# Kernel tuning notes

Hardware: AMD Instinct MI355X
Metric: run time of the kernel (lower is better)

The kernel has to match this reference:

```python
import jax, jax.numpy as jnp
import numpy as np

F = 128          # nbr_fea_len
A = 64           # angle_fea_len
N_EDGES = 100_000
N_ANGLES = 400_000
N_CRYST = 512
EPS = 1e-5
INV_SQRT_2 = 1.0 / 2.0 ** 0.5


def layer_norm(x, g, b):
    mu = jnp.mean(x, axis=-1, keepdims=True)
    var = jnp.var(x, axis=-1, keepdims=True)
    return (x - mu) * jax.lax.rsqrt(var + EPS) * g + b


def setup_inputs() -> dict:
    key = jax.random.key(0)
    ks = jax.random.split(key, 16)
    def lin(k, out_f, in_f):
        return (jax.random.normal(k, (out_f, in_f), jnp.float32) * (1.0 / np.sqrt(in_f))).astype(jnp.float32)
    return {
        "nbr_fea": jax.random.normal(ks[0], (N_EDGES, F), jnp.float32),
        "angle_fea": jax.random.normal(ks[1], (N_ANGLES, A), jnp.float32),
        "angle_nbr_idx": jax.random.randint(ks[2], (N_ANGLES, 2), 0, N_EDGES),
        "crystal_edge_idx": jax.random.randint(ks[3], (N_EDGES,), 0, N_CRYST),
        "crystal_angle_index": jnp.sort(jax.random.randint(ks[4], (N_ANGLES,), 0, N_CRYST)),
        "W_full": lin(ks[5], 2 * F, 2 * F + A),
        "W_mask": lin(ks[6], 1, F),
        "cn_gamma": jnp.ones((2 * F,), jnp.float32),
        "cn_beta": jnp.zeros((2 * F,), jnp.float32),
        "ln_core_g": jnp.ones((F,), jnp.float32),
        "ln_core_b": jnp.zeros((F,), jnp.float32),
        "ln2_g": jnp.ones((F,), jnp.float32),
        "ln2_b": jnp.zeros((F,), jnp.float32),
        "res_W1a": lin(ks[7], F // 2, F), "res_b1a": jnp.zeros((F // 2,), jnp.float32),
        "res_W2a": lin(ks[8], F, F // 2), "res_b2a": jnp.zeros((F,), jnp.float32),
        "res_W1b": lin(ks[9], F // 2, F), "res_b1b": jnp.zeros((F // 2,), jnp.float32),
        "res_W2b": lin(ks[10], F, F // 2), "res_b2b": jnp.zeros((F,), jnp.float32),
    }


def reference(nbr_fea, angle_fea, angle_nbr_idx, crystal_edge_idx, crystal_angle_index,
              W_full, W_mask, cn_gamma, cn_beta, ln_core_g, ln_core_b, ln2_g, ln2_b,
              res_W1a, res_b1a, res_W2a, res_b2a, res_W1b, res_b1b, res_W2b, res_b2b):
    source_idx = angle_nbr_idx[:, 0]
    # gather the two neighbor edge features per angle -> [n_angles, 2F]
    pair = nbr_fea[angle_nbr_idx].reshape(-1, 2 * F)
    total = jnp.concatenate([angle_fea, pair], axis=1)          # [n_angles, 2F+A]
    h = total @ W_full.T                                        # [n_angles, 2F]

    # Crystal_Norm: per-crystal, per-feature normalization over angle rows
    seg = crystal_angle_index
    cnt = jnp.maximum(jax.ops.segment_sum(jnp.ones((h.shape[0], 1), h.dtype), seg, N_CRYST), 1.0)
    mean = jax.ops.segment_sum(h, seg, N_CRYST) / cnt
    diff = h - mean[seg]
    var = jax.ops.segment_sum(diff * diff, seg, N_CRYST) / cnt
    h = diff * jax.lax.rsqrt(var + EPS)[seg] * cn_gamma + cn_beta

    nbr_core, nbr_filter = h[:, :F], h[:, F:]
    nbr_core = jax.nn.silu(layer_norm(nbr_core, ln_core_g, ln_core_b))
    gate = jax.nn.sigmoid(nbr_filter @ W_mask.T)                # [n_angles, 1]
    msg = gate * nbr_core

    # scatter-mean over source edge; empty edges get 0 (matches scatter+pad)
    s = jax.ops.segment_sum(msg, source_idx, N_EDGES)
    c = jax.ops.segment_sum(jnp.ones((msg.shape[0], 1), msg.dtype), source_idx, N_EDGES)
    nbr_sumed = s / jnp.maximum(c, 1.0)

    x = layer_norm(nbr_sumed, ln2_g, ln2_b)
    # two residual bottleneck blocks: x + fc2(silu(fc1(x)))
    x = x + (jax.nn.silu(x @ res_W1a.T + res_b1a) @ res_W2a.T + res_b2a)
    x = x + (jax.nn.silu(x @ res_W1b.T + res_b1b) @ res_W2b.T + res_b2b)
    return INV_SQRT_2 * (nbr_fea + x)
```

## Files before the change

kernel.cpp:

```cpp
#include <hip/hip_runtime.h>
#include <hip/hip_bf16.h>
#include <cstdint>
#include <cstddef>

#define NF 128
#define N_EDGES 100000
#define N_ANGLES 400000
#define N_CRYST 512
#define KDIM 320
#define TWOF 256
#define EPS_LN 1e-5f
#define INV_SQRT_2 0.70710678118654752440f

typedef short short8 __attribute__((ext_vector_type(8)));
typedef float floatx4 __attribute__((ext_vector_type(4)));

__device__ inline unsigned short f2bf(float x) {
    __hip_bfloat16 b = __float2bfloat16(x);
    return *reinterpret_cast<unsigned short*>(&b);
}
__device__ inline float bf2f(__hip_bfloat16 b) { return __bfloat162float(b); }
__device__ inline float bfbits2f(unsigned short u) {
    unsigned int v = ((unsigned int)u) << 16;
    return __uint_as_float(v);
}

__device__ inline uint4 cvt8(float4 a, float4 b) {
    __hip_bfloat162 p0 = __float22bfloat162_rn(make_float2(a.x, a.y));
    __hip_bfloat162 p1 = __float22bfloat162_rn(make_float2(a.z, a.w));
    __hip_bfloat162 p2 = __float22bfloat162_rn(make_float2(b.x, b.y));
    __hip_bfloat162 p3 = __float22bfloat162_rn(make_float2(b.z, b.w));
    uint4 r;
    r.x = *reinterpret_cast<unsigned int*>(&p0);
    r.y = *reinterpret_cast<unsigned int*>(&p1);
    r.z = *reinterpret_cast<unsigned int*>(&p2);
    r.w = *reinterpret_cast<unsigned int*>(&p3);
    return r;
}

__global__ void seg_bounds(const int* __restrict__ seg, int* __restrict__ seg_start) {
    int s = blockIdx.x * blockDim.x + threadIdx.x;
    if (s > N_CRYST) return;
    if (s == N_CRYST) { seg_start[N_CRYST] = N_ANGLES; return; }
    int lo = 0, hi = N_ANGLES;
    while (lo < hi) { int mid = (lo + hi) >> 1; if (seg[mid] < s) lo = mid + 1; else hi = mid; }
    seg_start[s] = lo;
}

__global__ __launch_bounds__(512) void gemm_gather_mfma(
    const float* __restrict__ angle_fea,
    const float* __restrict__ nbr_fea,
    const int*   __restrict__ angle_nbr_idx,
    const float* __restrict__ W_full,
    __hip_bfloat16* __restrict__ hout)
{
    __shared__ uint4 X_lds[512];
    __shared__ uint4 W_lds[1024];

    const int tid  = threadIdx.x;
    const int row0 = blockIdx.x * 128;

    const int xm = tid >> 2;
    const int xk = ((tid & 3) ^ ((xm >> 1) & 3)) * 8;
    const int p0 = angle_nbr_idx[(size_t)(row0 + xm) * 2 + 0];
    const int p1 = angle_nbr_idx[(size_t)(row0 + xm) * 2 + 1];
    int wn[2], wk[2];
    #pragma unroll
    for (int it = 0; it < 2; ++it) {
        int tau = it * 512 + tid;
        wn[it] = tau >> 2;
        wk[it] = ((tau & 3) ^ ((wn[it] >> 1) & 3)) * 8;
    }

    const int wave = tid >> 6, lane = tid & 63;
    const int wrow = (wave & 1) * 64;
    const int wcol = (wave >> 1) * 64;
    const int rl   = lane & 15, kgrp = lane >> 4;
    const int fragoff = (kgrp ^ ((rl >> 1) & 3)) * 16;
    const char* Xb = (const char*)X_lds;
    const char* Wb = (const char*)W_lds;

    floatx4 acc[4][4];
    #pragma unroll
    for (int i = 0; i < 4; ++i)
        #pragma unroll
        for (int j = 0; j < 4; ++j)
            acc[i][j] = (floatx4){0.f, 0.f, 0.f, 0.f};

    float4 xa, xb2, wa0, wb0, wa1, wb1;
    auto loadX = [&](int kbase, float4& a, float4& b) {
        const float* src;
        if (kbase < 64)       src = angle_fea + (size_t)(row0 + xm) * 64 + kbase + xk;
        else if (kbase < 192) src = nbr_fea + (size_t)p0 * 128 + (kbase - 64) + xk;
        else                  src = nbr_fea + (size_t)p1 * 128 + (kbase - 192) + xk;
        a = ((const float4*)src)[0];
        b = ((const float4*)src)[1];
    };
    auto loadW = [&](int kbase, int it, float4& a, float4& b) {
        const float* src = W_full + (size_t)wn[it] * KDIM + kbase + wk[it];
        a = ((const float4*)src)[0];
        b = ((const float4*)src)[1];
    };

    loadX(0, xa, xb2);
    loadW(0, 0, wa0, wb0);
    loadW(0, 1, wa1, wb1);

    #pragma unroll
    for (int kiter = 0; kiter < 10; ++kiter) {
        uint4 xc  = cvt8(xa, xb2);
        uint4 wc0 = cvt8(wa0, wb0);
        uint4 wc1 = cvt8(wa1, wb1);
        if (kiter > 0) __syncthreads();
        X_lds[tid]       = xc;
        W_lds[tid]       = wc0;
        W_lds[512 + tid] = wc1;
        __syncthreads();
        if (kiter < 9) {
            int nb = (kiter + 1) * 32;
            loadX(nb, xa, xb2);
            loadW(nb, 0, wa0, wb0);
            loadW(nb, 1, wa1, wb1);
        }
        short8 wf[4], xf[4];
        #pragma unroll
        for (int i = 0; i < 4; ++i)
            wf[i] = *(const short8*)(Wb + (size_t)(wcol + i * 16 + rl) * 64 + fragoff);
        #pragma unroll
        for (int j = 0; j < 4; ++j)
            xf[j] = *(const short8*)(Xb + (size_t)(wrow + j * 16 + rl) * 64 + fragoff);
        #pragma unroll
        for (int i = 0; i < 4; ++i)
            #pragma unroll
            for (int j = 0; j < 4; ++j)
                acc[i][j] = __builtin_amdgcn_mfma_f32_16x16x32_bf16(wf[i], xf[j], acc[i][j], 0, 0, 0);
    }

    unsigned short* hp = reinterpret_cast<unsigned short*>(hout);
    #pragma unroll
    for (int j = 0; j < 4; ++j) {
        size_t r = (size_t)(row0 + wrow + j * 16 + rl);
        #pragma unroll
        for (int i = 0; i < 4; ++i) {
            int c = wcol + i * 16 + kgrp * 4;
            floatx4 v = acc[i][j];
            uint2 pk;
            pk.x = (unsigned int)f2bf(v[0]) | ((unsigned int)f2bf(v[1]) << 16);
            pk.y = (unsigned int)f2bf(v[2]) | ((unsigned int)f2bf(v[3]) << 16);
            *reinterpret_cast<uint2*>(hp + r * TWOF + c) = pk;
        }
    }
}

__global__ __launch_bounds__(256) void seg_stats(
    const __hip_bfloat16* __restrict__ h,
    const int* __restrict__ seg_start,
    float* __restrict__ segSum, float* __restrict__ segSumSq)
{
    __shared__ float redS[8][256];
    __shared__ float redQ[8][256];
    int seg   = blockIdx.x;
    int split = blockIdx.y;
    int start = seg_start[seg], end = seg_start[seg + 1];
    int n = end - start;
    int g = threadIdx.x >> 5, t = threadIdx.x & 31;
    float s[8] = {0.f,0.f,0.f,0.f,0.f,0.f,0.f,0.f};
    float q[8] = {0.f,0.f,0.f,0.f,0.f,0.f,0.f,0.f};
    if (n > 0) {
        int per = (n + 3) >> 2;
        int r0 = start + split * per;
        int r1 = min(r0 + per, end);
        const unsigned short* hp = (const unsigned short*)h;
        for (int r = r0 + g; r < r1; r += 8) {
            uint4 v = *(const uint4*)(hp + (size_t)r * TWOF + t * 8);
            unsigned int d[4] = {v.x, v.y, v.z, v.w};
            #pragma unroll
            for (int i = 0; i < 4; ++i) {
                float lo = __uint_as_float(d[i] << 16);
                float hi = __uint_as_float(d[i] & 0xffff0000u);
                s[2*i]   += lo; q[2*i]   += lo * lo;
                s[2*i+1] += hi; q[2*i+1] += hi * hi;
            }
        }
    }
    #pragma unroll
    for (int i = 0; i < 8; ++i) { redS[g][t * 8 + i] = s[i]; redQ[g][t * 8 + i] = q[i]; }
    __syncthreads();
    if (n > 0) {
        int col = threadIdx.x;
        float S = 0.f, Q = 0.f;
        #pragma unroll
        for (int gg = 0; gg < 8; ++gg) { S += redS[gg][col]; Q += redQ[gg][col]; }
        atomicAdd(&segSum[seg * TWOF + col], S);
        atomicAdd(&segSumSq[seg * TWOF + col], Q);
    }
}

__global__ __launch_bounds__(256) void seg_finalize(
    const int* __restrict__ seg_start,
    float* __restrict__ segSum, float* __restrict__ segSumSq)
{
    int seg = blockIdx.x;
    int j = threadIdx.x;
    float cnt = (float)max(seg_start[seg + 1] - seg_start[seg], 1);
    float inv = 1.0f / cnt;
    float mean = segSum[seg * TWOF + j] * inv;
    float var  = segSumSq[seg * TWOF + j] * inv - mean * mean;
    segSum[seg * TWOF + j]   = mean;
    segSumSq[seg * TWOF + j] = rsqrtf(var + EPS_LN);
}

__global__ __launch_bounds__(256) void angle_msg(
    const __hip_bfloat16* __restrict__ h,
    const int* __restrict__ seg_idx,
    const int* __restrict__ angle_nbr_idx,
    const float* __restrict__ segMean, const float* __restrict__ segScale,
    const float* __restrict__ cn_gamma, const float* __restrict__ cn_beta,
    const float* __restrict__ ln_g, const float* __restrict__ ln_b,
    const float* __restrict__ w_mask,
    float* __restrict__ s_acc, float* __restrict__ c_acc)
{
    int row  = blockIdx.x * 4 + (threadIdx.x >> 6);
    int lane = threadIdx.x & 63;
    int seg  = seg_idx[row];
    int src  = angle_nbr_idx[(size_t)row * 2];

    const __hip_bfloat16* hr = h + (size_t)row * TWOF;
    float y[4];
    #pragma unroll
    for (int qq = 0; qq < 4; ++qq) {
        int col = lane + qq * 64;
        float v = bf2f(hr[col]);
        float m = segMean[seg * TWOF + col], sc = segScale[seg * TWOF + col];
        y[qq] = (v - m) * sc * cn_gamma[col] + cn_beta[col];
    }
    float sum = y[0] + y[1], ssq = y[0] * y[0] + y[1] * y[1];
    #pragma unroll
    for (int o = 32; o > 0; o >>= 1) { sum += __shfl_xor(sum, o, 64); ssq += __shfl_xor(ssq, o, 64); }
    float mu  = sum * (1.f / 128.f);
    float var = ssq * (1.f / 128.f) - mu * mu;
    float rs  = rsqrtf(var + EPS_LN);
    float ln0 = (y[0] - mu) * rs * ln_g[lane]      + ln_b[lane];
    float ln1 = (y[1] - mu) * rs * ln_g[lane + 64] + ln_b[lane + 64];
    float si0 = ln0 / (1.f + __expf(-ln0));
    float si1 = ln1 / (1.f + __expf(-ln1));
    float gp = y[2] * w_mask[lane] + y[3] * w_mask[lane + 64];
    #pragma unroll
    for (int o = 32; o > 0; o >>= 1) gp += __shfl_xor(gp, o, 64);
    float gate = 1.f / (1.f + __expf(-gp));

    atomicAdd(&s_acc[(size_t)src * NF + lane],      gate * si0);
    atomicAdd(&s_acc[(size_t)src * NF + lane + 64], gate * si1);
    if (lane == 0) atomicAdd(&c_acc[src], 1.0f);
}

#define MT 64
#define XBS 136
#define H1S 72
#define W1S 136
#define W2S 72
__global__ __launch_bounds__(256) void edge_mlp_mfma(
    const float* __restrict__ s_acc, const float* __restrict__ c_acc,
    const float* __restrict__ nbr_fea,
    const float* __restrict__ ln2_g, const float* __restrict__ ln2_b,
    const float* __restrict__ W1a, const float* __restrict__ b1a,
    const float* __restrict__ W2a, const float* __restrict__ b2a,
    const float* __restrict__ W1b, const float* __restrict__ b1b,
    const float* __restrict__ W2b, const float* __restrict__ b2b,
    float* __restrict__ out)
{
    __shared__ unsigned short xb[MT * XBS];
    __shared__ unsigned short h1[MT * H1S];
    __shared__ unsigned short wl[128 * W2S];

    const int tid  = threadIdx.x;
    const int row0 = blockIdx.x * MT;
    const int w    = tid >> 6, lane = tid & 63;
    const int rl   = lane & 15, kgrp = lane >> 4;

    {
        int m = tid >> 2;
        int q = tid & 3;
        int e = min(row0 + m, N_EDGES - 1);
        float inv = 1.f / fmaxf(c_acc[e], 1.f);
        const float4* src = (const float4*)(s_acc + (size_t)e * NF + q * 32);
        float v[32];
        float sum = 0.f, ssq = 0.f;
        #pragma unroll
        for (int t = 0; t < 8; ++t) {
            float4 f = src[t];
            v[4*t+0] = f.x * inv; v[4*t+1] = f.y * inv; v[4*t+2] = f.z * inv; v[4*t+3] = f.w * inv;
        }
        #pragma unroll
        for (int i = 0; i < 32; ++i) { sum += v[i]; ssq += v[i] * v[i]; }
        sum += __shfl_xor(sum, 1, 64); ssq += __shfl_xor(ssq, 1, 64);
        sum += __shfl_xor(sum, 2, 64); ssq += __shfl_xor(ssq, 2, 64);
        float mu  = sum * (1.f / 128.f);
        float var = ssq * (1.f / 128.f) - mu * mu;
        float rs  = rsqrtf(var + EPS_LN);
        #pragma unroll
        for (int i = 0; i < 32; ++i) {
            int col = q * 32 + i;
            v[i] = (v[i] - mu) * rs * ln2_g[col] + ln2_b[col];
        }
        #pragma unroll
        for (int t = 0; t < 4; ++t) {
            float4 a = make_float4(v[8*t+0], v[8*t+1], v[8*t+2], v[8*t+3]);
            float4 b = make_float4(v[8*t+4], v[8*t+5], v[8*t+6], v[8*t+7]);
            *(uint4*)&xb[m * XBS + q * 32 + t * 8] = cvt8(a, b);
        }
    }

    const float* W1s[2] = {W1a, W1b};
    const float* B1s[2] = {b1a, b1b};
    const float* W2s[2] = {W2a, W2b};
    const float* B2s[2] = {b2a, b2b};

    #pragma unroll 1
    for (int blk = 0; blk < 2; ++blk) {
        const float* W1 = W1s[blk]; const float* B1 = B1s[blk];
        const float* W2 = W2s[blk]; const float* B2 = B2s[blk];

        __syncthreads();
        #pragma unroll
        for (int c = tid; c < 1024; c += 256) {
            int nn = c >> 4, kc = c & 15;
            const float* src = W1 + (size_t)nn * 128 + kc * 8;
            *(uint4*)&wl[nn * W1S + kc * 8] =
                cvt8(((const float4*)src)[0], ((const float4*)src)[1]);
        }
        __syncthreads();

        short8 xf[4];
        #pragma unroll
        for (int ks = 0; ks < 4; ++ks)
            xf[ks] = *(const short8*)&xb[(w * 16 + rl) * XBS + ks * 32 + kgrp * 8];
        floatx4 a1[4];
        #pragma unroll
        for (int i = 0; i < 4; ++i) {
            a1[i] = (floatx4){0.f, 0.f, 0.f, 0.f};
            #pragma unroll
            for (int ks = 0; ks < 4; ++ks) {
                short8 wf = *(const short8*)&wl[(i * 16 + rl) * W1S + ks * 32 + kgrp * 8];
                a1[i] = __builtin_amdgcn_mfma_f32_16x16x32_bf16(wf, xf[ks], a1[i], 0, 0, 0);
            }
        }
        #pragma unroll
        for (int i = 0; i < 4; ++i) {
            int nb = i * 16 + kgrp * 4;
            float s0 = a1[i][0] + B1[nb + 0];
            float s1 = a1[i][1] + B1[nb + 1];
            float s2 = a1[i][2] + B1[nb + 2];
            float s3 = a1[i][3] + B1[nb + 3];
            s0 = s0 / (1.f + __expf(-s0));
            s1 = s1 / (1.f + __expf(-s1));
            s2 = s2 / (1.f + __expf(-s2));
            s3 = s3 / (1.f + __expf(-s3));
            unsigned int lo = (unsigned int)f2bf(s0) | ((unsigned int)f2bf(s1) << 16);
            unsigned int hi = (unsigned int)f2bf(s2) | ((unsigned int)f2bf(s3) << 16);
            *(unsigned int*)&h1[(w * 16 + rl) * H1S + nb]     = lo;
            *(unsigned int*)&h1[(w * 16 + rl) * H1S + nb + 2] = hi;
        }

        __syncthreads();
        #pragma unroll
        for (int c = tid; c < 1024; c += 256) {
            int pp = c >> 3, kc = c & 7;
            const float* src = W2 + (size_t)pp * 64 + kc * 8;
            *(uint4*)&wl[pp * W2S + kc * 8] =
                cvt8(((const float4*)src)[0], ((const float4*)src)[1]);
        }
        __syncthreads();

        short8 hf[2];
        #pragma unroll
        for (int ks = 0; ks < 2; ++ks)
            hf[ks] = *(const short8*)&h1[(w * 16 + rl) * H1S + ks * 32 + kgrp * 8];
        #pragma unroll
        for (int p = 0; p < 8; ++p) {
            floatx4 a2 = (floatx4){0.f, 0.f, 0.f, 0.f};
            #pragma unroll
            for (int ks = 0; ks < 2; ++ks) {
                short8 wf = *(const short8*)&wl[(p * 16 + rl) * W2S + ks * 32 + kgrp * 8];
                a2 = __builtin_amdgcn_mfma_f32_16x16x32_bf16(wf, hf[ks], a2, 0, 0, 0);
            }
            int m = w * 16 + rl;
            #pragma unroll
            for (int reg = 0; reg < 4; ++reg) {
                int pcol = p * 16 + kgrp * 4 + reg;
                int idx  = m * XBS + pcol;
                float xv = bfbits2f(xb[idx]);
                xb[idx] = f2bf(xv + a2[reg] + B2[pcol]);
            }
        }
    }

    {
        int m = tid >> 2;
        int q = tid & 3;
        int e = row0 + m;
        if (e < N_EDGES) {
            const float4* nf = (const float4*)(nbr_fea + (size_t)e * NF + q * 32);
            float4* dst      = (float4*)(out + (size_t)e * NF + q * 32);
            #pragma unroll
            for (int t = 0; t < 8; ++t) {
                float4 f = nf[t];
                int col = q * 32 + 4 * t;
                dst[t] = make_float4(
                    INV_SQRT_2 * (f.x + bfbits2f(xb[m * XBS + col + 0])),
                    INV_SQRT_2 * (f.y + bfbits2f(xb[m * XBS + col + 1])),
                    INV_SQRT_2 * (f.z + bfbits2f(xb[m * XBS + col + 2])),
                    INV_SQRT_2 * (f.w + bfbits2f(xb[m * XBS + col + 3])));
            }
        }
    }
}


extern "C" void kernel_launch(void* const* d_in, const int* in_sizes, int n_in,
                              void* d_out, int out_size, void* d_ws, size_t ws_size,
                              hipStream_t stream) {
    const float* nbr_fea       = (const float*)d_in[0];
    const float* angle_fea     = (const float*)d_in[1];
    const int*   angle_nbr_idx = (const int*)d_in[2];
    const int*   cai           = (const int*)d_in[4];
    const float* W_full        = (const float*)d_in[5];
    const float* W_mask        = (const float*)d_in[6];
    const float* cn_gamma      = (const float*)d_in[7];
    const float* cn_beta       = (const float*)d_in[8];
    const float* ln_core_g     = (const float*)d_in[9];
    const float* ln_core_b     = (const float*)d_in[10];
    const float* ln2_g         = (const float*)d_in[11];
    const float* ln2_b         = (const float*)d_in[12];
    const float* W1a           = (const float*)d_in[13];
    const float* b1a           = (const float*)d_in[14];
    const float* W2a           = (const float*)d_in[15];
    const float* b2a           = (const float*)d_in[16];
    const float* W1b           = (const float*)d_in[17];
    const float* b1b           = (const float*)d_in[18];
    const float* W2b           = (const float*)d_in[19];
    const float* b2b           = (const float*)d_in[20];
    float* out = (float*)d_out;

    char* ws = (char*)d_ws;
    float* segSum    = (float*)(ws + 0);
    float* segSumSq  = (float*)(ws + 524288);
    float* s_acc     = (float*)(ws + 1048576);
    float* c_acc     = (float*)(ws + 52248576);
    int*   seg_start = (int*)  (ws + 52648576);
    __hip_bfloat16* h = (__hip_bfloat16*)(ws + 52652672);

    hipMemsetAsync(ws, 0, 52648576, stream);

    seg_bounds<<<3, 256, 0, stream>>>(cai, seg_start);
    gemm_gather_mfma<<<N_ANGLES / 128, 512, 0, stream>>>(
        angle_fea, nbr_fea, angle_nbr_idx, W_full, h);
    seg_stats<<<dim3(N_CRYST, 4), 256, 0, stream>>>(h, seg_start, segSum, segSumSq);
    seg_finalize<<<N_CRYST, 256, 0, stream>>>(seg_start, segSum, segSumSq);
    angle_msg<<<N_ANGLES / 4, 256, 0, stream>>>(
        h, cai, angle_nbr_idx, segSum, segSumSq,
        cn_gamma, cn_beta, ln_core_g, ln_core_b, W_mask, s_acc, c_acc);
    edge_mlp_mfma<<<(N_EDGES + MT - 1) / MT, 256, 0, stream>>>(
        s_acc, c_acc, nbr_fea, ln2_g, ln2_b,
        W1a, b1a, W2a, b2a, W1b, b1b, W2b, b2b, out);
}
```

Before: 689.7 us.

## Prepack W to bf16, preload gathered X tile, double-buffer W in GEMM

Adds a small kernel that converts W_full to swizzled bf16 once per call, so the GEMM no longer converts weights in every block. The GEMM now uses 64-row tiles with 256 threads. Each block loads and converts its whole gathered X tile (all K) into LDS up front, then streams prepacked W through a double-buffered LDS slot with one barrier per k-step. Separately, angle_msg is vectorized: each lane reads 4 bf16 values and float4 parameters, and the LayerNorm and gate reductions are split across half-waves. The cost is more LDS per block, which may lower occupancy, and W traffic doubles relative to the number of rows.

```diff
diff --git a/kernel.cpp b/kernel.cpp
--- a/kernel.cpp
+++ b/kernel.cpp
@@ -38,6 +38,17 @@
     return r;
 }
 
+__global__ __launch_bounds__(256) void w_pack(const float* __restrict__ W_full,
+                                              uint4* __restrict__ wsW) {
+    int s  = blockIdx.x * 256 + threadIdx.x;
+    int ki = s >> 10;
+    int sl = s & 1023;
+    int n  = sl >> 2, kc = sl & 3;
+    int ko = (kc ^ ((n >> 1) & 3)) * 8;
+    const float* src = W_full + (size_t)n * KDIM + ki * 32 + ko;
+    wsW[s] = cvt8(((const float4*)src)[0], ((const float4*)src)[1]);
+}
+
 __global__ void seg_bounds(const int* __restrict__ seg, int* __restrict__ seg_start) {
     int s = blockIdx.x * blockDim.x + threadIdx.x;
     if (s > N_CRYST) return;
@@ -47,38 +58,53 @@
     seg_start[s] = lo;
 }
 
-__global__ __launch_bounds__(512) void gemm_gather_mfma(
+__global__ __launch_bounds__(256) void gemm_gather_mfma(
     const float* __restrict__ angle_fea,
     const float* __restrict__ nbr_fea,
     const int*   __restrict__ angle_nbr_idx,
-    const float* __restrict__ W_full,
+    const uint4* __restrict__ wsW,
     __hip_bfloat16* __restrict__ hout)
 {
-    __shared__ uint4 X_lds[512];
-    __shared__ uint4 W_lds[1024];
+    __shared__ uint4 X_lds[2560];
+    __shared__ uint4 W_lds[2][1024];
 
     const int tid  = threadIdx.x;
-    const int row0 = blockIdx.x * 128;
+    const int row0 = blockIdx.x * 64;
 
     const int xm = tid >> 2;
-    const int xk = ((tid & 3) ^ ((xm >> 1) & 3)) * 8;
+    const int xko = ((tid & 3) ^ ((xm >> 1) & 3)) * 8;
     const int p0 = angle_nbr_idx[(size_t)(row0 + xm) * 2 + 0];
     const int p1 = angle_nbr_idx[(size_t)(row0 + xm) * 2 + 1];
-    int wn[2], wk[2];
-    #pragma unroll
-    for (int it = 0; it < 2; ++it) {
-        int tau = it * 512 + tid;
-        wn[it] = tau >> 2;
-        wk[it] = ((tau & 3) ^ ((wn[it] >> 1) & 3)) * 8;
-    }
+
+    float4 ra[10], rb[10];
+    #pragma unroll
+    for (int ki = 0; ki < 10; ++ki) {
+        const int kb = ki * 32;
+        const float* src;
+        if (kb < 64)       src = angle_fea + (size_t)(row0 + xm) * 64 + kb + xko;
+        else if (kb < 192) src = nbr_fea + (size_t)p0 * 128 + (kb - 64) + xko;
+        else               src = nbr_fea + (size_t)p1 * 128 + (kb - 192) + xko;
+        ra[ki] = ((const float4*)src)[0];
+        rb[ki] = ((const float4*)src)[1];
+    }
+    #pragma unroll
+    for (int ki = 0; ki < 10; ++ki)
+        X_lds[ki * 256 + tid] = cvt8(ra[ki], rb[ki]);
+
+    {
+        uint4 w0[4];
+        #pragma unroll
+        for (int it = 0; it < 4; ++it) w0[it] = wsW[it * 256 + tid];
+        #pragma unroll
+        for (int it = 0; it < 4; ++it) W_lds[0][it * 256 + tid] = w0[it];
+    }
+    __syncthreads();
 
     const int wave = tid >> 6, lane = tid & 63;
-    const int wrow = (wave & 1) * 64;
-    const int wcol = (wave >> 1) * 64;
+    const int wcol = wave * 64;
     const int rl   = lane & 15, kgrp = lane >> 4;
     const int fragoff = (kgrp ^ ((rl >> 1) & 3)) * 16;
     const char* Xb = (const char*)X_lds;
-    const char* Wb = (const char*)W_lds;
 
     floatx4 acc[4][4];
     #pragma unroll
@@ -87,59 +113,39 @@
         for (int j = 0; j < 4; ++j)
             acc[i][j] = (floatx4){0.f, 0.f, 0.f, 0.f};
 
-    float4 xa, xb2, wa0, wb0, wa1, wb1;
-    auto loadX = [&](int kbase, float4& a, float4& b) {
-        const float* src;
-        if (kbase < 64)       src = angle_fea + (size_t)(row0 + xm) * 64 + kbase + xk;
-        else if (kbase < 192) src = nbr_fea + (size_t)p0 * 128 + (kbase - 64) + xk;
-        else                  src = nbr_fea + (size_t)p1 * 128 + (kbase - 192) + xk;
-        a = ((const float4*)src)[0];
-        b = ((const float4*)src)[1];
-    };
-    auto loadW = [&](int kbase, int it, float4& a, float4& b) {
-        const float* src = W_full + (size_t)wn[it] * KDIM + kbase + wk[it];
-        a = ((const float4*)src)[0];
-        b = ((const float4*)src)[1];
-    };
-
-    loadX(0, xa, xb2);
-    loadW(0, 0, wa0, wb0);
-    loadW(0, 1, wa1, wb1);
-
-    #pragma unroll
-    for (int kiter = 0; kiter < 10; ++kiter) {
-        uint4 xc  = cvt8(xa, xb2);
-        uint4 wc0 = cvt8(wa0, wb0);
-        uint4 wc1 = cvt8(wa1, wb1);
-        if (kiter > 0) __syncthreads();
-        X_lds[tid]       = xc;
-        W_lds[tid]       = wc0;
-        W_lds[512 + tid] = wc1;
-        __syncthreads();
-        if (kiter < 9) {
-            int nb = (kiter + 1) * 32;
-            loadX(nb, xa, xb2);
-            loadW(nb, 0, wa0, wb0);
-            loadW(nb, 1, wa1, wb1);
-        }
+    #pragma unroll
+    for (int ki = 0; ki < 10; ++ki) {
+        uint4 wnext[4];
+        if (ki < 9) {
+            #pragma unroll
+            for (int it = 0; it < 4; ++it)
+                wnext[it] = wsW[(ki + 1) * 1024 + it * 256 + tid];
+        }
+        const char* Wb = (const char*)&W_lds[ki & 1][0];
         short8 wf[4], xf[4];
         #pragma unroll
         for (int i = 0; i < 4; ++i)
             wf[i] = *(const short8*)(Wb + (size_t)(wcol + i * 16 + rl) * 64 + fragoff);
         #pragma unroll
         for (int j = 0; j < 4; ++j)
-            xf[j] = *(const short8*)(Xb + (size_t)(wrow + j * 16 + rl) * 64 + fragoff);
+            xf[j] = *(const short8*)(Xb + (size_t)ki * 4096 + (size_t)(j * 16 + rl) * 64 + fragoff);
         #pragma unroll
         for (int i = 0; i < 4; ++i)
             #pragma unroll
             for (int j = 0; j < 4; ++j)
                 acc[i][j] = __builtin_amdgcn_mfma_f32_16x16x32_bf16(wf[i], xf[j], acc[i][j], 0, 0, 0);
+        if (ki < 9) {
+            #pragma unroll
+            for (int it = 0; it < 4; ++it)
+                W_lds[(ki + 1) & 1][it * 256 + tid] = wnext[it];
+            __syncthreads();
+        }
     }
 
     unsigned short* hp = reinterpret_cast<unsigned short*>(hout);
     #pragma unroll
     for (int j = 0; j < 4; ++j) {
-        size_t r = (size_t)(row0 + wrow + j * 16 + rl);
+        size_t r = (size_t)(row0 + j * 16 + rl);
         #pragma unroll
         for (int i = 0; i < 4; ++i) {
             int c = wcol + i * 16 + kgrp * 4;
@@ -224,34 +230,60 @@
     int lane = threadIdx.x & 63;
     int seg  = seg_idx[row];
     int src  = angle_nbr_idx[(size_t)row * 2];
-
-    const __hip_bfloat16* hr = h + (size_t)row * TWOF;
+    int c4   = lane * 4;
+
+    uint2 hv = *(const uint2*)((const unsigned short*)h + (size_t)row * TWOF + c4);
     float y[4];
-    #pragma unroll
-    for (int qq = 0; qq < 4; ++qq) {
-        int col = lane + qq * 64;
-        float v = bf2f(hr[col]);
-        float m = segMean[seg * TWOF + col], sc = segScale[seg * TWOF + col];
-        y[qq] = (v - m) * sc * cn_gamma[col] + cn_beta[col];
-    }
-    float sum = y[0] + y[1], ssq = y[0] * y[0] + y[1] * y[1];
-    #pragma unroll
-    for (int o = 32; o > 0; o >>= 1) { sum += __shfl_xor(sum, o, 64); ssq += __shfl_xor(ssq, o, 64); }
-    float mu  = sum * (1.f / 128.f);
-    float var = ssq * (1.f / 128.f) - mu * mu;
-    float rs  = rsqrtf(var + EPS_LN);
-    float ln0 = (y[0] - mu) * rs * ln_g[lane]      + ln_b[lane];
-    float ln1 = (y[1] - mu) * rs * ln_g[lane + 64] + ln_b[lane + 64];
-    float si0 = ln0 / (1.f + __expf(-ln0));
-    float si1 = ln1 / (1.f + __expf(-ln1));
-    float gp = y[2] * w_mask[lane] + y[3] * w_mask[lane + 64];
-    #pragma unroll
-    for (int o = 32; o > 0; o >>= 1) gp += __shfl_xor(gp, o, 64);
-    float gate = 1.f / (1.f + __expf(-gp));
-
-    atomicAdd(&s_acc[(size_t)src * NF + lane],      gate * si0);
-    atomicAdd(&s_acc[(size_t)src * NF + lane + 64], gate * si1);
-    if (lane == 0) atomicAdd(&c_acc[src], 1.0f);
+    y[0] = __uint_as_float(hv.x << 16);
+    y[1] = __uint_as_float(hv.x & 0xffff0000u);
+    y[2] = __uint_as_float(hv.y << 16);
+    y[3] = __uint_as_float(hv.y & 0xffff0000u);
+
+    float4 m4 = *(const float4*)&segMean[seg * TWOF + c4];
+    float4 s4 = *(const float4*)&segScale[seg * TWOF + c4];
+    float4 g4 = *(const float4*)&cn_gamma[c4];
+    float4 b4 = *(const float4*)&cn_beta[c4];
+    y[0] = (y[0] - m4.x) * s4.x * g4.x + b4.x;
+    y[1] = (y[1] - m4.y) * s4.y * g4.y + b4.y;
+    y[2] = (y[2] - m4.z) * s4.z * g4.z + b4.z;
+    y[3] = (y[3] - m4.w) * s4.w * g4.w + b4.w;
+
+    float sum, ssq, gp;
+    if (lane < 32) {
+        sum = y[0] + y[1] + y[2] + y[3];
+        ssq = y[0]*y[0] + y[1]*y[1] + y[2]*y[2] + y[3]*y[3];
+        gp  = 0.f;
+    } else {
+        float4 wm = *(const float4*)&w_mask[c4 - 128];
+        gp  = y[0]*wm.x + y[1]*wm.y + y[2]*wm.z + y[3]*wm.w;
+        sum = 0.f; ssq = 0.f;
+    }
+    #pragma unroll
+    for (int o = 16; o > 0; o >>= 1) {
+        sum += __shfl_xor(sum, o, 64);
+        ssq += __shfl_xor(ssq, o, 64);
+        gp  += __shfl_xor(gp,  o, 64);
+    }
+    float gate = 1.f / (1.f + __expf(-__shfl(gp, 32, 64)));
+
+    if (lane < 32) {
+        float mu  = sum * (1.f / 128.f);
+        float var = ssq * (1.f / 128.f) - mu * mu;
+        float rs  = rsqrtf(var + EPS_LN);
+        float4 lg = *(const float4*)&ln_g[c4];
+        float4 lb = *(const float4*)&ln_b[c4];
+        float l0 = (y[0] - mu) * rs * lg.x + lb.x;
+        float l1 = (y[1] - mu) * rs * lg.y + lb.y;
+        float l2 = (y[2] - mu) * rs * lg.z + lb.z;
+        float l3 = (y[3] - mu) * rs * lg.w + lb.w;
+        float* d = &s_acc[(size_t)src * NF + c4];
+        atomicAdd(d + 0, gate * (l0 / (1.f + __expf(-l0))));
+        atomicAdd(d + 1, gate * (l1 / (1.f + __expf(-l1))));
+        atomicAdd(d + 2, gate * (l2 / (1.f + __expf(-l2))));
+        atomicAdd(d + 3, gate * (l3 / (1.f + __expf(-l3))));
+    } else if (lane == 32) {
+        atomicAdd(&c_acc[src], 1.0f);
+    }
 }
 
 #define MT 64
@@ -449,12 +481,14 @@
     float* c_acc     = (float*)(ws + 52248576);
     int*   seg_start = (int*)  (ws + 52648576);
     __hip_bfloat16* h = (__hip_bfloat16*)(ws + 52652672);
+    uint4* wsW       = (uint4*)(ws + 257452672);
 
     hipMemsetAsync(ws, 0, 52648576, stream);
 
+    w_pack<<<40, 256, 0, stream>>>(W_full, wsW);
     seg_bounds<<<3, 256, 0, stream>>>(cai, seg_start);
-    gemm_gather_mfma<<<N_ANGLES / 128, 512, 0, stream>>>(
-        angle_fea, nbr_fea, angle_nbr_idx, W_full, h);
+    gemm_gather_mfma<<<N_ANGLES / 64, 256, 0, stream>>>(
+        angle_fea, nbr_fea, angle_nbr_idx, wsW, h);
     seg_stats<<<dim3(N_CRYST, 4), 256, 0, stream>>>(h, seg_start, segSum, segSumSq);
     seg_finalize<<<N_CRYST, 256, 0, stream>>>(seg_start, segSum, segSumSq);
     angle_msg<<<N_ANGLES / 4, 256, 0, stream>>>(
```

New measurement: 1.203 ms. 1.74x slower.
